# Kernel tuning notes

Measured on AMD Instinct MI355X. Metric: run time of the kernel, lower is better.

The kernel has to match this reference:

```python
import jax, jax.numpy as jnp
import numpy as np

ROUTINGS = 3

def squash(x):
    # x: [..., O]; squash along last dim
    norm = jnp.linalg.norm(x, axis=-1, keepdims=True)
    scale = norm ** 2 / (1 + norm ** 2) / (norm + 1e-9)
    return scale * x

def setup_inputs() -> dict:
    key = jax.random.key(0)
    k1, k2 = jax.random.split(key)
    B, K, I, O, C = 256, 10, 1152, 16, 8
    x = jax.random.normal(k1, (B, I, C), dtype=jnp.float32)
    w = jax.random.normal(k2, (K, I, O, C), dtype=jnp.float32) * 0.05
    return {"x": x, "w": w}

def reference(x, w):
    # x: [B, I, Cin], w: [K, I, O, Cin]
    # u_hat[b,k,i,o] = sum_c w[k,i,o,c] * x[b,i,c]
    u_hat = jnp.einsum('kioc,bic->bkio', w, x)  # [B, K, I, O]
    B, K, I, O = u_hat.shape
    b = jnp.zeros((B, K, I, 1), dtype=u_hat.dtype)
    # routing iterations (fixed small loop); intermediate iters use detached u_hat
    u_hat_d = jax.lax.stop_gradient(u_hat)
    for _ in range(ROUTINGS - 1):
        c = jax.nn.softmax(b, axis=1)              # softmax over output capsules K
        s = jnp.sum(c * u_hat_d, axis=2)           # [B, K, O]
        v = squash(s)                              # [B, K, O]
        uv = jnp.einsum('bkio,bko->bki', u_hat_d, v)[..., None]  # [B, K, I, 1]
        b = b + uv
    c = jax.nn.softmax(b, axis=1)
    s = jnp.sum(c * u_hat, axis=2)
    v = squash(s)
    return v  # [B, K, O]
```

## Files before the change

kernel.cpp:

```cpp
#include <hip/hip_runtime.h>

#define B_ 256
#define K_ 10
#define I_ 1152
#define O_ 16
#define C_ 8
#define BKO (B_*K_*O_)
#define NX 72

static __device__ __forceinline__ unsigned short f32_bf16(float f) {
    unsigned int u = __float_as_uint(f);
    u += 0x7FFFu + ((u >> 16) & 1u);
    return (unsigned short)(u >> 16);
}

template <int CTRL>
static __device__ __forceinline__ float dpp_add(float v) {
    int x = __builtin_amdgcn_update_dpp(0, __float_as_int(v), CTRL, 0xF, 0xF, true);
    return v + __int_as_float(x);
}
static __device__ __forceinline__ float row16_sum(float v) {
    v = dpp_add<0xB1>(v);
    v = dpp_add<0x4E>(v);
    v = dpp_add<0x141>(v);
    v = dpp_add<0x140>(v);
    return v;
}
static __device__ __forceinline__ float quad8_sum(float v) {
    v = dpp_add<0xB1>(v);
    v = dpp_add<0x4E>(v);
    v = dpp_add<0x141>(v);
    return v;
}

__global__ __launch_bounds__(256) void uhat_kernel(
    const float* __restrict__ x, const float* __restrict__ w,
    unsigned short* __restrict__ u, float* __restrict__ part)
{
    __shared__ float w_lds[16 * 132];
    __shared__ float p_lds[64 * 17];
    const int t   = threadIdx.x;
    const int i_l = t & 15, tg = t >> 4;
    const int i0  = blockIdx.x * 16;
    const int b0  = blockIdx.y * 64 + tg * 4;
    const int k   = blockIdx.z;
    const int i   = i0 + i_l;
    const bool row_leader = (i_l == 0);

    float4 xr[4][2];
#pragma unroll
    for (int bb = 0; bb < 4; bb++) {
        const float4* xp = (const float4*)(x + ((size_t)(b0 + bb) * I_ + i) * C_);
        xr[bb][0] = xp[0];
        xr[bb][1] = xp[1];
    }

    {
        const float4* ws = (const float4*)(w + ((size_t)k * I_ + i0) * O_ * C_);
#pragma unroll
        for (int r = 0; r < 2; r++) {
            int idx = r * 256 + t;
            int ii = idx >> 5, rem = idx & 31;
            *(float4*)&w_lds[ii * 132 + rem * 4] = ws[idx];
        }
    }
    __syncthreads();

    unsigned int pk[4][8];
#pragma unroll
    for (int oo = 0; oo < 8; oo++) {
        float d[4][2];
#pragma unroll
        for (int h = 0; h < 2; h++) {
            const int o = oo * 2 + h;
            const float4 w0 = *(const float4*)&w_lds[i_l * 132 + o * 8];
            const float4 w1 = *(const float4*)&w_lds[i_l * 132 + o * 8 + 4];
#pragma unroll
            for (int bb = 0; bb < 4; bb++) {
                d[bb][h] = w0.x*xr[bb][0].x + w0.y*xr[bb][0].y
                         + w0.z*xr[bb][0].z + w0.w*xr[bb][0].w
                         + w1.x*xr[bb][1].x + w1.y*xr[bb][1].y
                         + w1.z*xr[bb][1].z + w1.w*xr[bb][1].w;
            }
        }
#pragma unroll
        for (int bb = 0; bb < 4; bb++) {
#pragma unroll
            for (int h = 0; h < 2; h++) {
                const float rs = row16_sum(d[bb][h]);
                if (row_leader)
                    p_lds[(tg * 4 + bb) * 17 + oo * 2 + h] = rs;
            }
        }
#pragma unroll
        for (int bb = 0; bb < 4; bb++)
            pk[bb][oo] = (unsigned int)f32_bf16(d[bb][0]) |
                         ((unsigned int)f32_bf16(d[bb][1]) << 16);
    }
#pragma unroll
    for (int bb = 0; bb < 4; bb++) {
        unsigned int* dst = (unsigned int*)
            (u + (((size_t)(b0 + bb) * K_ + k) * I_ + i) * O_);
        *(uint4*)(dst)     = make_uint4(pk[bb][0], pk[bb][1], pk[bb][2], pk[bb][3]);
        *(uint4*)(dst + 4) = make_uint4(pk[bb][4], pk[bb][5], pk[bb][6], pk[bb][7]);
    }

    __syncthreads();
    {
        const int bl = t >> 2, o4 = (t & 3) * 4;
        float4 v;
        v.x = p_lds[bl * 17 + o4 + 0];
        v.y = p_lds[bl * 17 + o4 + 1];
        v.z = p_lds[bl * 17 + o4 + 2];
        v.w = p_lds[bl * 17 + o4 + 3];
        *(float4*)&part[(((size_t)blockIdx.x * K_ + k) * 256
                         + blockIdx.y * 64 + bl) * O_ + o4] = v;
    }
}

static __device__ __forceinline__ void sweep(
    const char* __restrict__ ubb,
    int i_l, int og, const float* __restrict__ v_lds, float acc[K_][2])
{
#pragma unroll
    for (int k = 0; k < K_; k++) { acc[k][0] = 0.f; acc[k][1] = 0.f; }

    const int base = i_l * 32 + og * 4;

    unsigned int P[K_], Q[K_];
#pragma unroll
    for (int k = 0; k < K_; k++)
        P[k] = *(const unsigned int*)(ubb + k * 36864 + base);

#pragma unroll 1
    for (int ic = 0; ic < 9; ic++) {
        if (ic + 1 < 9) {
#pragma unroll
            for (int k = 0; k < K_; k++)
                Q[k] = *(const unsigned int*)
                    (ubb + k * 36864 + (ic + 1) * 4096 + base);
        }
        float c_[K_];
        float Z = 0.f;
#pragma unroll
        for (int k = 0; k < K_; k++) {
            const float f0 = __uint_as_float(P[k] << 16);
            const float f1 = __uint_as_float(P[k] & 0xffff0000u);
            const float2 vk = *(const float2*)&v_lds[k * 16 + og * 2];
            float lk = f0 * vk.x + f1 * vk.y;
            lk = quad8_sum(lk);
            c_[k] = __expf(lk); Z += c_[k];
        }
        const float inv = 1.0f / Z;
#pragma unroll
        for (int k = 0; k < K_; k++) {
            const float ck = c_[k] * inv;
            acc[k][0] = fmaf(ck, __uint_as_float(P[k] << 16),         acc[k][0]);
            acc[k][1] = fmaf(ck, __uint_as_float(P[k] & 0xffff0000u), acc[k][1]);
        }
#pragma unroll
        for (int k = 0; k < K_; k++) P[k] = Q[k];
    }
}

static __device__ __forceinline__ void block_reduce(
    float acc[K_][2], float* __restrict__ red, int lane, int wv)
{
#pragma unroll
    for (int k = 0; k < K_; k++)
#pragma unroll
        for (int j = 0; j < 2; j++) {
            float a = acc[k][j];
            a += __shfl_xor(a, 8); a += __shfl_xor(a, 16); a += __shfl_xor(a, 32);
            acc[k][j] = a;
        }
    if (lane < 8) {
#pragma unroll
        for (int k = 0; k < K_; k++)
            *(float2*)&red[wv * 160 + k * 16 + lane * 2] =
                make_float2(acc[k][0], acc[k][1]);
    }
    __syncthreads();
}

static __device__ __forceinline__ float sum16(const float* __restrict__ red, int t)
{
    float s = 0.f;
#pragma unroll
    for (int wgi = 0; wgi < 16; wgi++) s += red[wgi * 160 + t];
    return s;
}

static __device__ __forceinline__ float squash_v(float s) {
    float n2 = s * s;
    n2 += __shfl_xor(n2, 1); n2 += __shfl_xor(n2, 2);
    n2 += __shfl_xor(n2, 4); n2 += __shfl_xor(n2, 8);
    const float norm = sqrtf(n2);
    return s * (n2 / (1.0f + n2) / (norm + 1e-9f));
}

__global__ __launch_bounds__(1024) void route_all(
    const unsigned short* __restrict__ u, const float* __restrict__ part,
    float* __restrict__ out)
{
    __shared__ float red[16 * 160];
    __shared__ float v_lds[160];
    __shared__ float v1_lds[160];

    const int t    = threadIdx.x;
    const int og   = t & 7, i_l = t >> 3;
    const int b    = blockIdx.x;
    const int lane = t & 63, wv = t >> 6;

    const char* ubb = (const char*)(u + (size_t)b * K_ * I_ * O_);
    float acc[K_][2];

    if (t < 160) {
        const int k = t >> 4, o = t & 15;
        const float* pb = part + ((size_t)k * 256 + b) * O_ + o;
        float s = 0.f;
#pragma unroll
        for (int xb = 0; xb < NX; xb++)
            s += pb[(size_t)xb * BKO];
        float v = squash_v(s * (1.0f / K_));
        v1_lds[t] = v;
        v_lds[t]  = v;
    }
    __syncthreads();

    sweep(ubb, i_l, og, v_lds, acc);
    block_reduce(acc, red, lane, wv);
    float v12 = 0.f;
    if (t < 160) v12 = v1_lds[t] + squash_v(sum16(red, t));
    __syncthreads();
    if (t < 160) v_lds[t] = v12;
    __syncthreads();

    sweep(ubb, i_l, og, v_lds, acc);
    block_reduce(acc, red, lane, wv);
    if (t < 160)
        out[(size_t)b * 160 + t] = squash_v(sum16(red, t));
}

extern "C" void kernel_launch(void* const* d_in, const int* in_sizes, int n_in,
                              void* d_out, int out_size, void* d_ws, size_t ws_size,
                              hipStream_t stream)
{
    const float* x = (const float*)d_in[0];
    const float* w = (const float*)d_in[1];
    float* outp = (float*)d_out;

    float* part = (float*)d_ws;
    unsigned short* u = (unsigned short*)(part + (size_t)NX * BKO);

    uhat_kernel<<<dim3(72, 4, 10), 256, 0, stream>>>(x, w, u, part);
    route_all<<<B_, 1024, 0, stream>>>(u, part, outp);
}
```

Measured before the change: 123.1 us.

## Stage first three u_hat chunks into LDS during pass 2 for reuse in pass 3

During the first routing sweep, the first three i-chunks of each batch's bf16 u_hat are copied asynchronously into a 120 KB LDS buffer with global_load_lds. The final sweep then reads those chunks from LDS instead of global memory and streams only the rest. The goal is to cut global/L2 traffic in the second pass. The trade-off is heavy LDS use, which holds occupancy to one 1024-thread block per CU, and extra load instructions in pass 2.

```diff
diff --git a/kernel.cpp b/kernel.cpp
--- a/kernel.cpp
+++ b/kernel.cpp
@@ -118,12 +118,56 @@
     }
 }
 
-static __device__ __forceinline__ void sweep(
-    const char* __restrict__ ubb,
-    int i_l, int og, const float* __restrict__ v_lds, float acc[K_][2])
+
+static __device__ __forceinline__ void stage_chunk_1024(
+    const char* __restrict__ ubb, int chunk, int t, char* lds_buf)
+{
+    const size_t coff = (size_t)chunk * 4096;
+#pragma unroll
+    for (int r = 0; r < 3; r++) {
+        if (r < 2 || t < 512) {
+            const int L   = r * 1024 + t;
+            const int k   = L >> 8, rem = L & 255;
+            const char* src = ubb + (size_t)k * 36864 + coff + (size_t)rem * 16;
+            char* dst = lds_buf + ((size_t)(r * 1024 + (t & ~63)) * 16);
+            __builtin_amdgcn_global_load_lds(
+                (const __attribute__((address_space(1))) unsigned int*)src,
+                (__attribute__((address_space(3))) unsigned int*)dst,
+                16, 0, 0);
+        }
+    }
+}
+
+#define CHUNK_OG8(PP) do {                                                    \
+    float c_[K_]; float Z = 0.f;                                              \
+    _Pragma("unroll")                                                         \
+    for (int k = 0; k < K_; k++) {                                            \
+        const float f0 = __uint_as_float(PP[k] << 16);                        \
+        const float f1 = __uint_as_float(PP[k] & 0xffff0000u);                \
+        const float2 vk = *(const float2*)&v_lds[k * 16 + og * 2];            \
+        float lk = f0 * vk.x + f1 * vk.y;                                     \
+        lk = quad8_sum(lk);                                                   \
+        c_[k] = __expf(lk); Z += c_[k];                                       \
+    }                                                                         \
+    const float inv = 1.0f / Z;                                               \
+    _Pragma("unroll")                                                         \
+    for (int k = 0; k < K_; k++) {                                            \
+        const float ck = c_[k] * inv;                                         \
+        acc[k][0] = fmaf(ck, __uint_as_float(PP[k] << 16),         acc[k][0]);\
+        acc[k][1] = fmaf(ck, __uint_as_float(PP[k] & 0xffff0000u), acc[k][1]);\
+    }                                                                         \
+} while (0)
+
+static __device__ __forceinline__ void sweep_pass2(
+    const char* __restrict__ ubb, int t, int i_l, int og,
+    const float* __restrict__ v_lds, float acc[K_][2], char* __restrict__ ubuf)
 {
 #pragma unroll
     for (int k = 0; k < K_; k++) { acc[k][0] = 0.f; acc[k][1] = 0.f; }
+
+    stage_chunk_1024(ubb, 0, t, ubuf);
+    stage_chunk_1024(ubb, 1, t, ubuf + 40960);
+    stage_chunk_1024(ubb, 2, t, ubuf + 81920);
 
     const int base = i_l * 32 + og * 4;
 
@@ -140,24 +184,44 @@
                 Q[k] = *(const unsigned int*)
                     (ubb + k * 36864 + (ic + 1) * 4096 + base);
         }
-        float c_[K_];
-        float Z = 0.f;
-#pragma unroll
-        for (int k = 0; k < K_; k++) {
-            const float f0 = __uint_as_float(P[k] << 16);
-            const float f1 = __uint_as_float(P[k] & 0xffff0000u);
-            const float2 vk = *(const float2*)&v_lds[k * 16 + og * 2];
-            float lk = f0 * vk.x + f1 * vk.y;
-            lk = quad8_sum(lk);
-            c_[k] = __expf(lk); Z += c_[k];
-        }
-        const float inv = 1.0f / Z;
-#pragma unroll
-        for (int k = 0; k < K_; k++) {
-            const float ck = c_[k] * inv;
-            acc[k][0] = fmaf(ck, __uint_as_float(P[k] << 16),         acc[k][0]);
-            acc[k][1] = fmaf(ck, __uint_as_float(P[k] & 0xffff0000u), acc[k][1]);
-        }
+        CHUNK_OG8(P);
+#pragma unroll
+        for (int k = 0; k < K_; k++) P[k] = Q[k];
+    }
+}
+
+static __device__ __forceinline__ void sweep_pass3(
+    const char* __restrict__ ubb, int i_l, int og,
+    const float* __restrict__ v_lds, float acc[K_][2],
+    const char* __restrict__ ubuf)
+{
+#pragma unroll
+    for (int k = 0; k < K_; k++) { acc[k][0] = 0.f; acc[k][1] = 0.f; }
+
+    const int base = i_l * 32 + og * 4;
+
+#pragma unroll 1
+    for (int ic = 0; ic < 3; ic++) {
+        const char* cb = ubuf + (size_t)ic * 40960;
+        unsigned int P[K_];
+#pragma unroll
+        for (int k = 0; k < K_; k++)
+            P[k] = *(const unsigned int*)(cb + k * 4096 + base);
+        CHUNK_OG8(P);
+    }
+    unsigned int P[K_], Q[K_];
+#pragma unroll
+    for (int k = 0; k < K_; k++)
+        P[k] = *(const unsigned int*)(ubb + k * 36864 + 3 * 4096 + base);
+#pragma unroll 1
+    for (int ic = 3; ic < 9; ic++) {
+        if (ic + 1 < 9) {
+#pragma unroll
+            for (int k = 0; k < K_; k++)
+                Q[k] = *(const unsigned int*)
+                    (ubb + k * 36864 + (ic + 1) * 4096 + base);
+        }
+        CHUNK_OG8(P);
 #pragma unroll
         for (int k = 0; k < K_; k++) P[k] = Q[k];
     }
@@ -203,6 +267,7 @@
     const unsigned short* __restrict__ u, const float* __restrict__ part,
     float* __restrict__ out)
 {
+    __shared__ __align__(16) char ubuf[3 * 40960];
     __shared__ float red[16 * 160];
     __shared__ float v_lds[160];
     __shared__ float v1_lds[160];
@@ -228,7 +293,7 @@
     }
     __syncthreads();
 
-    sweep(ubb, i_l, og, v_lds, acc);
+    sweep_pass2(ubb, t, i_l, og, v_lds, acc, ubuf);
     block_reduce(acc, red, lane, wv);
     float v12 = 0.f;
     if (t < 160) v12 = v1_lds[t] + squash_v(sum16(red, t));
@@ -236,7 +301,7 @@
     if (t < 160) v_lds[t] = v12;
     __syncthreads();
 
-    sweep(ubb, i_l, og, v_lds, acc);
+    sweep_pass3(ubb, i_l, og, v_lds, acc, ubuf);
     block_reduce(acc, red, lane, wv);
     if (t < 160)
         out[(size_t)b * 160 + t] = squash_v(sum16(red, t));
```

Result: no change. 121.0 us (-1.8%).
